# Optimization experiments

Hardware: AMD Instinct MI355X
Metric: run time of the kernel (lower is better)

The kernel has to match this reference:

```python
import jax, jax.numpy as jnp
import numpy as np

B, L, D, H = 4, 2048, 1024, 16
HD = D // H  # head_dim = 64


def setup_inputs() -> dict:
    key = jax.random.key(0)
    k1, k2, k3, k4 = jax.random.split(key, 4)
    x = jax.random.normal(k1, (B, L, D), dtype=jnp.float32)
    key_padding_mask = jax.random.randint(k2, (B, L), 0, 2) == 1
    scale = 1.0 / np.sqrt(D)
    Wqkv = jax.random.normal(k3, (3 * D, D), dtype=jnp.float32) * scale
    Wproj = jax.random.normal(k4, (D, D), dtype=jnp.float32) * scale
    return {"x": x, "key_padding_mask": key_padding_mask, "Wqkv": Wqkv, "Wproj": Wproj}


def reference(x, key_padding_mask, Wqkv, Wproj):
    b, l, d = x.shape
    qkv = jnp.einsum('bld,ed->ble', x, Wqkv)          # [B, L, 3D]
    q, k, v = jnp.split(qkv, 3, axis=-1)
    # [B, H, L, HD]
    q = q.reshape(b, l, H, HD).transpose(0, 2, 1, 3)
    k = k.reshape(b, l, H, HD).transpose(0, 2, 1, 3)
    v = v.reshape(b, l, H, HD).transpose(0, 2, 1, 3)
    scale = 1.0 / jnp.sqrt(jnp.asarray(HD, dtype=x.dtype))
    scores = jnp.einsum('bhqd,bhkd->bhqk', q, k) * scale  # [B, H, L, L]
    # key_padding_mask True = PAD -> -inf bias on key axis
    bias = jnp.where(key_padding_mask[:, None, None, :], -jnp.inf, 0.0).astype(x.dtype)
    attn = jax.nn.softmax(scores + bias, axis=-1)
    y = jnp.einsum('bhqk,bhkd->bhqd', attn, v)            # [B, H, L, HD]
    y = y.transpose(0, 2, 1, 3).reshape(b, l, d)          # [B, L, D]
    return jnp.einsum('bld,ed->ble', y, Wproj)
```

## Files before the change

### kernel.cpp

```cpp
#include <hip/hip_runtime.h>

#define L_SEQ 2048
#define DIM   1024
#define NH    16
#define HDIM  64
#define KDIM  1024

typedef short  short8 __attribute__((ext_vector_type(8)));
typedef __bf16 bf16x8 __attribute__((ext_vector_type(8)));
typedef __bf16 bf16x4 __attribute__((ext_vector_type(4)));
typedef float  f32x4  __attribute__((ext_vector_type(4)));
typedef unsigned u32x4 __attribute__((ext_vector_type(4)));

__device__ __forceinline__ unsigned short f2bf(float f) {
  unsigned u = __builtin_bit_cast(unsigned, f);
  u += 0x7fffu + ((u >> 16) & 1u);
  return (unsigned short)(u >> 16);
}

__device__ __forceinline__ void gload16(const void* g, void* l) {
  __builtin_amdgcn_global_load_lds(
      (const __attribute__((address_space(1))) void*)g,
      (__attribute__((address_space(3))) void*)l, 16, 0, 0);
}

__device__ __forceinline__ bf16x8 ldfrag(const unsigned short* p) {
  return __builtin_bit_cast(bf16x8, *(const short8*)p);
}
#define MFMA16(a, b, c) __builtin_amdgcn_mfma_f32_16x16x32_bf16(a, b, c, 0, 0, 0)

__device__ __forceinline__ unsigned cvtpk(float a, float b) {
  unsigned r;
  asm("v_cvt_pk_bf16_f32 %0, %1, %2" : "=v"(r) : "v"(a), "v"(b));
  return r;
}
__device__ __forceinline__ void xchg(unsigned &a, unsigned &b) {
  asm("v_permlane32_swap_b32 %0, %1" : "+v"(a), "+v"(b));
  asm("v_permlane16_swap_b32 %0, %1" : "+v"(a), "+v"(b));
}

__global__ __launch_bounds__(256) void cvt_bf16(const float* __restrict__ src,
                                                unsigned short* __restrict__ dst,
                                                int n) {
  int i = (blockIdx.x * 256 + threadIdx.x) * 8;
  if (i >= n) return;
  f32x4 a = *(const f32x4*)(src + i);
  f32x4 b = *(const f32x4*)(src + i + 4);
  short8 o;
  o[0] = (short)f2bf(a[0]); o[1] = (short)f2bf(a[1]);
  o[2] = (short)f2bf(a[2]); o[3] = (short)f2bf(a[3]);
  o[4] = (short)f2bf(b[0]); o[5] = (short)f2bf(b[1]);
  o[6] = (short)f2bf(b[2]); o[7] = (short)f2bf(b[3]);
  *(short8*)(dst + i) = o;
}

__global__ __launch_bounds__(256) void zero_buf(f32x4* __restrict__ dst, int n4) {
  int i = blockIdx.x * 256 + threadIdx.x;
  if (i < n4) dst[i] = f32x4{0.f, 0.f, 0.f, 0.f};
}

__global__ __launch_bounds__(256) void mask_scan(const int* __restrict__ mask,
                                                 int* __restrict__ rowl,
                                                 int* __restrict__ lc) {
  const int b = blockIdx.x, t = threadIdx.x;
  __shared__ int wsum[4];
  __shared__ int lcs;
  const int* mrow = mask + b * L_SEQ + t * 8;
  int m[8], c = 0;
#pragma unroll
  for (int i = 0; i < 8; ++i) { m[i] = mrow[i]; c += (m[i] == 0); }
  const int lane = t & 63, w = t >> 6;
  int sc = c;
#pragma unroll
  for (int d = 1; d < 64; d <<= 1) {
    int v = __shfl_up(sc, d);
    if (lane >= d) sc += v;
  }
  if (lane == 63) wsum[w] = sc;
  __syncthreads();
  int pre = sc - c;
  for (int i = 0; i < w; ++i) pre += wsum[i];
  int run = pre;
#pragma unroll
  for (int i = 0; i < 8; ++i) {
    if (m[i] == 0) { rowl[b * L_SEQ + run] = t * 8 + i; ++run; }
  }
  if (t == 255) { lc[b] = run; lcs = run; }
  __syncthreads();
  int total = lcs;
#pragma unroll
  for (int i = 0; i < 8; ++i) {
    int slot = t * 8 + i;
    if (slot >= total) rowl[b * L_SEQ + slot] = 0;
  }
}

__device__ __forceinline__ void gemm128_mainloop(
    const unsigned short* __restrict__ A, const unsigned short* __restrict__ Bt,
    const int (&asrc)[4], int n0,
    unsigned short* As0, unsigned short* As1,
    unsigned short* Bs0, unsigned short* Bs1,
    f32x4 (&acc)[4][4]) {
  const int t = threadIdx.x;
  const int lane = t & 63, wid = t >> 6;
  const int wm = wid >> 1, wn = wid & 1;
  const int lr = lane & 15, lk = (lane >> 4) * 8;
  const int swr = (lr & 7) << 3;
  constexpr int NT = KDIM / 64;

  auto stage = [&](unsigned short* Ad, unsigned short* Bd, int kt) {
#pragma unroll
    for (int i = 0; i < 4; ++i) {
      int row = i * 32 + (t >> 3);
      int cs = ((t & 7) ^ (row & 7)) * 8;
      gload16(A + (size_t)asrc[i] * KDIM + kt * 64 + cs,
              Ad + row * 64 + (t & 7) * 8);
    }
#pragma unroll
    for (int i = 0; i < 4; ++i) {
      int row = i * 32 + (t >> 3);
      int cs = ((t & 7) ^ (row & 7)) * 8;
      gload16(Bt + (size_t)(n0 + row) * KDIM + kt * 64 + cs,
              Bd + row * 64 + (t & 7) * 8);
    }
  };

  auto tile = [&](const unsigned short* Ac, const unsigned short* Bc,
                  unsigned short* An, unsigned short* Bn, int kt) {
    if (kt + 1 < NT) {
      stage(An, Bn, kt + 1);
      asm volatile("s_waitcnt vmcnt(8)" ::: "memory");
    } else {
      asm volatile("s_waitcnt vmcnt(0)" ::: "memory");
    }
    __builtin_amdgcn_sched_barrier(0);
    __builtin_amdgcn_s_barrier();
    __builtin_amdgcn_sched_barrier(0);
    bf16x8 af[4][2], bfv[4][2];
#pragma unroll
    for (int mf = 0; mf < 4; ++mf)
#pragma unroll
      for (int kh = 0; kh < 2; ++kh)
        af[mf][kh] = ldfrag(Ac + (wm * 64 + mf * 16 + lr) * 64 +
                            ((kh * 32 + lk) ^ swr));
#pragma unroll
    for (int nf = 0; nf < 4; ++nf)
#pragma unroll
      for (int kh = 0; kh < 2; ++kh)
        bfv[nf][kh] = ldfrag(Bc + (wn * 64 + nf * 16 + lr) * 64 +
                             ((kh * 32 + lk) ^ swr));
    __builtin_amdgcn_s_setprio(1);
#pragma unroll
    for (int mf = 0; mf < 4; ++mf)
#pragma unroll
      for (int nf = 0; nf < 4; ++nf) {
        acc[mf][nf] = MFMA16(af[mf][0], bfv[nf][0], acc[mf][nf]);
        acc[mf][nf] = MFMA16(af[mf][1], bfv[nf][1], acc[mf][nf]);
      }
    __builtin_amdgcn_s_setprio(0);
    __builtin_amdgcn_sched_barrier(0);
    __builtin_amdgcn_s_barrier();
  };

  stage(As0, Bs0, 0);
  for (int kt = 0; kt < NT; kt += 2) {
    tile(As0, Bs0, As1, Bs1, kt);
    tile(As1, Bs1, As0, Bs0, kt + 1);
  }
}

__global__ __launch_bounds__(256, 2) void gemm_qkv(
    const unsigned short* __restrict__ xb, const unsigned short* __restrict__ wb,
    const int* __restrict__ rowl, const int* __restrict__ lc,
    unsigned short* __restrict__ qw, unsigned short* __restrict__ kw,
    unsigned short* __restrict__ vtw) {
  __shared__ unsigned short As[2][128 * 64];
  __shared__ unsigned short Bs[2][128 * 64];
  const int nx = blockIdx.x;
  const int m0 = blockIdx.y * 128;
  const int sec = nx >> 3;
  const int n0 = nx * 128;
  const int b = m0 >> 11;
  const int lcb = lc[b];
  if (sec > 0 && (m0 & 2047) >= lcb) return;
  const int t = threadIdx.x;
  int asrc[4];
#pragma unroll
  for (int i = 0; i < 4; ++i) {
    int p = m0 + i * 32 + (t >> 3);
    asrc[i] = (sec == 0) ? p : ((p & ~2047) + rowl[p]);
  }
  f32x4 acc[4][4] = {};
  gemm128_mainloop(xb, wb, asrc, n0, As[0], As[1], Bs[0], Bs[1], acc);

  const int lane = t & 63, wid = t >> 6;
  const int wm = wid >> 1, wn = wid & 1;
  const int lr = lane & 15, g4 = (lane >> 4) * 4;
  const int nb = n0 & 1023;
  if (sec == 0) {
#pragma unroll
    for (int mf = 0; mf < 4; ++mf)
#pragma unroll
      for (int nf = 0; nf < 4; ++nf) {
        int e = nb + wn * 64 + nf * 16 + lr;
        int h = e >> 6, hd = e & 63;
#pragma unroll
        for (int r = 0; r < 4; ++r) {
          int m = m0 + wm * 64 + mf * 16 + g4 + r;
          qw[(((size_t)(b * NH + h)) * L_SEQ + (m & 2047)) * HDIM + hd] =
              f2bf(acc[mf][nf][r]);
        }
      }
  } else {
#pragma unroll
    for (int mf = 0; mf < 4; ++mf)
#pragma unroll
      for (int r = 0; r < 4; ++r) {
        int m = m0 + wm * 64 + mf * 16 + g4 + r;
        int tgt = m & 2047;
        if (tgt >= lcb) continue;
        size_t bb = (size_t)b * NH;
#pragma unroll
        for (int nf = 0; nf < 4; ++nf) {
          int e = nb + wn * 64 + nf * 16 + lr;
          int h = e >> 6, hd = e & 63;
          unsigned short val = f2bf(acc[mf][nf][r]);
          if (sec == 1) kw[((bb + h) * L_SEQ + tgt) * HDIM + hd] = val;
          else          vtw[((bb + h) * HDIM + hd) * L_SEQ + tgt] = val;
        }
      }
  }
}

__global__ __launch_bounds__(256, 2) void gemm_proj(
    const unsigned short* __restrict__ yb, const unsigned short* __restrict__ wb,
    float* __restrict__ out) {
  __shared__ unsigned short As[2][128 * 64];
  __shared__ unsigned short Bs[2][128 * 64];
  const int n0 = blockIdx.x * 128, m0 = blockIdx.y * 128;
  const int t = threadIdx.x;
  int asrc[4];
#pragma unroll
  for (int i = 0; i < 4; ++i) asrc[i] = m0 + i * 32 + (t >> 3);
  f32x4 acc[4][4] = {};
  gemm128_mainloop(yb, wb, asrc, n0, As[0], As[1], Bs[0], Bs[1], acc);
  const int lane = t & 63, wid = t >> 6;
  const int wm = wid >> 1, wn = wid & 1;
  const int lr = lane & 15, g4 = (lane >> 4) * 4;
#pragma unroll
  for (int mf = 0; mf < 4; ++mf)
#pragma unroll
    for (int nf = 0; nf < 4; ++nf) {
      int e = n0 + wn * 64 + nf * 16 + lr;
#pragma unroll
      for (int r = 0; r < 4; ++r) {
        int m = m0 + wm * 64 + mf * 16 + g4 + r;
        out[(size_t)m * DIM + e] = acc[mf][nf][r];
      }
    }
}

__global__ __launch_bounds__(256, 4) void attn_kernel(
    const unsigned short* __restrict__ qw, const unsigned short* __restrict__ kw,
    const unsigned short* __restrict__ vtw, const int* __restrict__ lc,
    unsigned short* __restrict__ yb) {
  __shared__ unsigned short Ks[2][64 * 64];
  __shared__ unsigned short Vts[2][64 * 64];
  const int bh = blockIdx.y;
  const int q0 = blockIdx.x * 128;
  const int b = bh >> 4, h = bh & 15;
  const int t = threadIdx.x, wid = t >> 6, lane = t & 63;
  const int lr = lane & 15, lk = (lane >> 4) * 8, g4 = (lane >> 4) * 4;
  const int swr = (lr & 7) << 3;
  const float KE = 0.18033688011112042f;

  const int Lcv = lc[b];
  const int nt = (Lcv + 63) >> 6;

  bf16x8 qf[2][2];
  const size_t qbase = (size_t)bh * L_SEQ + q0 + wid * 32;
#pragma unroll
  for (int qi = 0; qi < 2; ++qi)
#pragma unroll
    for (int kh = 0; kh < 2; ++kh)
      qf[qi][kh] = __builtin_bit_cast(bf16x8,
          *(const short8*)(qw + (qbase + qi * 16 + lr) * HDIM + kh * 32 + lk));

  f32x4 o[2][4] = {};
  float mrun[2] = {-3.0e38f, -3.0e38f};
  float lrun[2] = {0.f, 0.f};

  auto stage = [&](int buf, int kt) {
#pragma unroll
    for (int i = 0; i < 2; ++i) {
      int c = i * 256 + t;
      int row = c >> 3;
      int cs = ((c & 7) ^ (row & 7)) * 8;
      gload16(kw  + ((size_t)bh * L_SEQ + kt * 64 + row) * HDIM + cs, &Ks[buf][c * 8]);
      gload16(vtw + ((size_t)bh * HDIM + row) * L_SEQ + kt * 64 + cs, &Vts[buf][c * 8]);
    }
  };

  stage(0, 0);
  int cur = 0;

  for (int kt = 0; kt < nt; ++kt) {
    if (kt + 1 < nt) {
      stage(cur ^ 1, kt + 1);
      asm volatile("s_waitcnt vmcnt(4)" ::: "memory");
    } else {
      asm volatile("s_waitcnt vmcnt(0)" ::: "memory");
    }
    __builtin_amdgcn_s_barrier();
    __builtin_amdgcn_sched_barrier(0);

    const unsigned short* Kc = Ks[cur];
    f32x4 s[2][4] = {};
    __builtin_amdgcn_s_setprio(1);
#pragma unroll
    for (int nf = 0; nf < 4; ++nf) {
      bf16x8 k0 = __builtin_bit_cast(bf16x8,
          *(const short8*)(Kc + (nf * 16 + lr) * 64 + ((0 + lk) ^ swr)));
      bf16x8 k1 = __builtin_bit_cast(bf16x8,
          *(const short8*)(Kc + (nf * 16 + lr) * 64 + ((32 + lk) ^ swr)));
      s[0][nf] = MFMA16(k0, qf[0][0], s[0][nf]);
      s[0][nf] = MFMA16(k1, qf[0][1], s[0][nf]);
      s[1][nf] = MFMA16(k0, qf[1][0], s[1][nf]);
      s[1][nf] = MFMA16(k1, qf[1][1], s[1][nf]);
    }
    __builtin_amdgcn_s_setprio(0);

    if (kt == nt - 1) {
      int kbase = kt * 64 + g4;
#pragma unroll
      for (int nf = 0; nf < 4; ++nf)
#pragma unroll
        for (int r = 0; r < 4; ++r)
          if (kbase + nf * 16 + r >= Lcv) {
            s[0][nf][r] = -3.0e38f;
            s[1][nf][r] = -3.0e38f;
          }
    }

    float pmax[2];
#pragma unroll
    for (int qi = 0; qi < 2; ++qi) {
      float a0 = fmaxf(fmaxf(s[qi][0][0], s[qi][0][1]), fmaxf(s[qi][0][2], s[qi][0][3]));
      float a1 = fmaxf(fmaxf(s[qi][1][0], s[qi][1][1]), fmaxf(s[qi][1][2], s[qi][1][3]));
      float a2 = fmaxf(fmaxf(s[qi][2][0], s[qi][2][1]), fmaxf(s[qi][2][2], s[qi][2][3]));
      float a3 = fmaxf(fmaxf(s[qi][3][0], s[qi][3][1]), fmaxf(s[qi][3][2], s[qi][3][3]));
      float mm = fmaxf(fmaxf(a0, a1), fmaxf(a2, a3));
      mm = fmaxf(mm, __shfl_xor(mm, 16));
      mm = fmaxf(mm, __shfl_xor(mm, 32));
      pmax[qi] = mm;
    }

    bool need = (pmax[0] > mrun[0] + 8.0f) || (pmax[1] > mrun[1] + 8.0f);
    if (__any(need)) {
#pragma unroll
      for (int qi = 0; qi < 2; ++qi) {
        float mn = fmaxf(mrun[qi], pmax[qi]);
        float al = __builtin_amdgcn_exp2f((mrun[qi] - mn) * KE);
        mrun[qi] = mn;
        lrun[qi] *= al;
#pragma unroll
        for (int df = 0; df < 4; ++df) o[qi][df] *= al;
      }
    }

    bf16x8 pb[2][2];
#pragma unroll
    for (int qi = 0; qi < 2; ++qi) {
      float mk_ = mrun[qi] * KE;
      f32x4 rs4 = {0.f, 0.f, 0.f, 0.f};
#pragma unroll
      for (int nf = 0; nf < 4; ++nf) {
#pragma unroll
        for (int r = 0; r < 4; ++r)
          s[qi][nf][r] = __builtin_amdgcn_exp2f(s[qi][nf][r] * KE - mk_);
        rs4 += s[qi][nf];
      }
      float rsum = (rs4[0] + rs4[1]) + (rs4[2] + rs4[3]);
      rsum += __shfl_xor(rsum, 16);
      rsum += __shfl_xor(rsum, 32);
      lrun[qi] += rsum;
      unsigned w00 = cvtpk(s[qi][0][0], s[qi][0][1]);
      unsigned w01 = cvtpk(s[qi][0][2], s[qi][0][3]);
      unsigned w10 = cvtpk(s[qi][1][0], s[qi][1][1]);
      unsigned w11 = cvtpk(s[qi][1][2], s[qi][1][3]);
      unsigned w20 = cvtpk(s[qi][2][0], s[qi][2][1]);
      unsigned w21 = cvtpk(s[qi][2][2], s[qi][2][3]);
      unsigned w30 = cvtpk(s[qi][3][0], s[qi][3][1]);
      unsigned w31 = cvtpk(s[qi][3][2], s[qi][3][3]);
      xchg(w00, w10);
      xchg(w01, w11);
      xchg(w20, w30);
      xchg(w21, w31);
      u32x4 f0 = {w00, w01, w10, w11};
      u32x4 f1 = {w20, w21, w30, w31};
      pb[qi][0] = __builtin_bit_cast(bf16x8, f0);
      pb[qi][1] = __builtin_bit_cast(bf16x8, f1);
    }

    const unsigned short* Vc = Vts[cur];
    __builtin_amdgcn_s_setprio(1);
#pragma unroll
    for (int df = 0; df < 4; ++df) {
      bf16x8 v0 = __builtin_bit_cast(bf16x8,
          *(const short8*)(Vc + (df * 16 + lr) * 64 + ((0 + lk) ^ swr)));
      bf16x8 v1 = __builtin_bit_cast(bf16x8,
          *(const short8*)(Vc + (df * 16 + lr) * 64 + ((32 + lk) ^ swr)));
      o[0][df] = MFMA16(v0, pb[0][0], o[0][df]);
      o[0][df] = MFMA16(v1, pb[0][1], o[0][df]);
      o[1][df] = MFMA16(v0, pb[1][0], o[1][df]);
      o[1][df] = MFMA16(v1, pb[1][1], o[1][df]);
    }
    __builtin_amdgcn_s_setprio(0);

    __builtin_amdgcn_sched_barrier(0);
    __builtin_amdgcn_s_barrier();
    cur ^= 1;
  }

#pragma unroll
  for (int qi = 0; qi < 2; ++qi) {
    float inv = 1.0f / lrun[qi];
    int q = q0 + wid * 32 + qi * 16 + lr;
#pragma unroll
    for (int df = 0; df < 4; ++df) {
      bf16x4 pk = {(__bf16)(o[qi][df][0] * inv), (__bf16)(o[qi][df][1] * inv),
                   (__bf16)(o[qi][df][2] * inv), (__bf16)(o[qi][df][3] * inv)};
      *(bf16x4*)(yb + ((size_t)b * L_SEQ + q) * DIM + h * 64 + df * 16 + g4) = pk;
    }
  }
}

extern "C" void kernel_launch(void* const* d_in, const int* in_sizes, int n_in,
                              void* d_out, int out_size, void* d_ws, size_t ws_size,
                              hipStream_t stream) {
  const float* x     = (const float*)d_in[0];
  const int*   mask  = (const int*)d_in[1];
  const float* wqkv  = (const float*)d_in[2];
  const float* wproj = (const float*)d_in[3];
  char* ws = (char*)d_ws;
  unsigned short* xb     = (unsigned short*)(ws + 0);
  unsigned short* wqkvb  = (unsigned short*)(ws + 16777216);
  unsigned short* wprojb = (unsigned short*)(ws + 23068672);
  unsigned short* qw     = (unsigned short*)(ws + 25165824);
  unsigned short* kw     = (unsigned short*)(ws + 41943040);
  unsigned short* vtw    = (unsigned short*)(ws + 58720256);
  unsigned short* yb     = (unsigned short*)(ws + 75497472);
  int*            rowl   = (int*)(ws + 92274688);
  int*            lcArr  = (int*)(ws + 92307456);

  cvt_bf16<<<dim3(8388608 / 2048), 256, 0, stream>>>(x, xb, 8388608);
  cvt_bf16<<<dim3(3145728 / 2048), 256, 0, stream>>>(wqkv, wqkvb, 3145728);
  cvt_bf16<<<dim3(1048576 / 2048), 256, 0, stream>>>(wproj, wprojb, 1048576);
  mask_scan<<<dim3(4), 256, 0, stream>>>(mask, rowl, lcArr);
  zero_buf<<<dim3(4096), 256, 0, stream>>>((f32x4*)vtw, 1048576);
  gemm_qkv<<<dim3(24, 64), 256, 0, stream>>>(xb, wqkvb, rowl, lcArr, qw, kw, vtw);
  attn_kernel<<<dim3(16, 64), 256, 0, stream>>>(qw, kw, vtw, lcArr, yb);
  gemm_proj<<<dim3(8, 64), 256, 0, stream>>>(yb, wprojb, (float*)d_out);
}
```

Before: 166.4 us.

## Load GEMM B fragments directly from global, remap blocks across XCDs

The GEMM mainloop no longer stages the weight tile in LDS. Each wave reads its B fragments straight from global memory into registers, which halves LDS use and lets occupancy rise to 3 blocks per CU. The vmcnt waits are adjusted to count the extra in-flight loads. All three kernels also get a block-index swizzle that groups neighbouring tiles on the same XCD for L2 locality. The risk is less-coalesced global reads for B, since each lane fetches 16-byte chunks from rows spaced KDIM apart, and possible register pressure.

Result: slower. 230.9 us (+38.8%).

```diff
diff --git a/kernel.cpp b/kernel.cpp
--- a/kernel.cpp
+++ b/kernel.cpp
@@ -99,7 +99,6 @@
     const unsigned short* __restrict__ A, const unsigned short* __restrict__ Bt,
     const int (&asrc)[4], int n0,
     unsigned short* As0, unsigned short* As1,
-    unsigned short* Bs0, unsigned short* Bs1,
     f32x4 (&acc)[4][4]) {
   const int t = threadIdx.x;
   const int lane = t & 63, wid = t >> 6;
@@ -108,7 +107,9 @@
   const int swr = (lr & 7) << 3;
   constexpr int NT = KDIM / 64;
 
-  auto stage = [&](unsigned short* Ad, unsigned short* Bd, int kt) {
+  const unsigned short* bbase = Bt + (size_t)(n0 + wn * 64 + lr) * KDIM + lk;
+
+  auto stageA = [&](unsigned short* Ad, int kt) {
 #pragma unroll
     for (int i = 0; i < 4; ++i) {
       int row = i * 32 + (t >> 3);
@@ -116,39 +117,32 @@
       gload16(A + (size_t)asrc[i] * KDIM + kt * 64 + cs,
               Ad + row * 64 + (t & 7) * 8);
     }
-#pragma unroll
-    for (int i = 0; i < 4; ++i) {
-      int row = i * 32 + (t >> 3);
-      int cs = ((t & 7) ^ (row & 7)) * 8;
-      gload16(Bt + (size_t)(n0 + row) * KDIM + kt * 64 + cs,
-              Bd + row * 64 + (t & 7) * 8);
-    }
   };
 
-  auto tile = [&](const unsigned short* Ac, const unsigned short* Bc,
-                  unsigned short* An, unsigned short* Bn, int kt) {
+  auto tile = [&](const unsigned short* Ac, unsigned short* An, int kt) {
+    bf16x8 bfv[4][2];
+#pragma unroll
+    for (int nf = 0; nf < 4; ++nf)
+#pragma unroll
+      for (int kh = 0; kh < 2; ++kh)
+        bfv[nf][kh] = __builtin_bit_cast(bf16x8,
+            *(const short8*)(bbase + nf * 16 * KDIM + kt * 64 + kh * 32));
     if (kt + 1 < NT) {
-      stage(An, Bn, kt + 1);
+      stageA(An, kt + 1);
+      asm volatile("s_waitcnt vmcnt(12)" ::: "memory");
+    } else {
       asm volatile("s_waitcnt vmcnt(8)" ::: "memory");
-    } else {
-      asm volatile("s_waitcnt vmcnt(0)" ::: "memory");
     }
     __builtin_amdgcn_sched_barrier(0);
     __builtin_amdgcn_s_barrier();
     __builtin_amdgcn_sched_barrier(0);
-    bf16x8 af[4][2], bfv[4][2];
+    bf16x8 af[4][2];
 #pragma unroll
     for (int mf = 0; mf < 4; ++mf)
 #pragma unroll
       for (int kh = 0; kh < 2; ++kh)
         af[mf][kh] = ldfrag(Ac + (wm * 64 + mf * 16 + lr) * 64 +
                             ((kh * 32 + lk) ^ swr));
-#pragma unroll
-    for (int nf = 0; nf < 4; ++nf)
-#pragma unroll
-      for (int kh = 0; kh < 2; ++kh)
-        bfv[nf][kh] = ldfrag(Bc + (wn * 64 + nf * 16 + lr) * 64 +
-                             ((kh * 32 + lk) ^ swr));
     __builtin_amdgcn_s_setprio(1);
 #pragma unroll
     for (int mf = 0; mf < 4; ++mf)
@@ -162,22 +156,23 @@
     __builtin_amdgcn_s_barrier();
   };
 
-  stage(As0, Bs0, 0);
+  stageA(As0, 0);
   for (int kt = 0; kt < NT; kt += 2) {
-    tile(As0, Bs0, As1, Bs1, kt);
-    tile(As1, Bs1, As0, Bs0, kt + 1);
-  }
-}
-
-__global__ __launch_bounds__(256, 2) void gemm_qkv(
+    tile(As0, As1, kt);
+    tile(As1, As0, kt + 1);
+  }
+}
+
+__global__ __launch_bounds__(256, 3) void gemm_qkv(
     const unsigned short* __restrict__ xb, const unsigned short* __restrict__ wb,
     const int* __restrict__ rowl, const int* __restrict__ lc,
     unsigned short* __restrict__ qw, unsigned short* __restrict__ kw,
     unsigned short* __restrict__ vtw) {
   __shared__ unsigned short As[2][128 * 64];
-  __shared__ unsigned short Bs[2][128 * 64];
-  const int nx = blockIdx.x;
-  const int m0 = blockIdx.y * 128;
+  const int flat = blockIdx.x + 24 * blockIdx.y;
+  const int e = (flat & 7) * 192 + (flat >> 3);
+  const int nx = e >> 6;
+  const int m0 = (e & 63) * 128;
   const int sec = nx >> 3;
   const int n0 = nx * 128;
   const int b = m0 >> 11;
@@ -191,7 +186,7 @@
     asrc[i] = (sec == 0) ? p : ((p & ~2047) + rowl[p]);
   }
   f32x4 acc[4][4] = {};
-  gemm128_mainloop(xb, wb, asrc, n0, As[0], As[1], Bs[0], Bs[1], acc);
+  gemm128_mainloop(xb, wb, asrc, n0, As[0], As[1], acc);
 
   const int lane = t & 63, wid = t >> 6;
   const int wm = wid >> 1, wn = wid & 1;
@@ -202,8 +197,8 @@
     for (int mf = 0; mf < 4; ++mf)
 #pragma unroll
       for (int nf = 0; nf < 4; ++nf) {
-        int e = nb + wn * 64 + nf * 16 + lr;
-        int h = e >> 6, hd = e & 63;
+        int e2 = nb + wn * 64 + nf * 16 + lr;
+        int h = e2 >> 6, hd = e2 & 63;
 #pragma unroll
         for (int r = 0; r < 4; ++r) {
           int m = m0 + wm * 64 + mf * 16 + g4 + r;
@@ -222,8 +217,8 @@
         size_t bb = (size_t)b * NH;
 #pragma unroll
         for (int nf = 0; nf < 4; ++nf) {
-          int e = nb + wn * 64 + nf * 16 + lr;
-          int h = e >> 6, hd = e & 63;
+          int e2 = nb + wn * 64 + nf * 16 + lr;
+          int h = e2 >> 6, hd = e2 & 63;
           unsigned short val = f2bf(acc[mf][nf][r]);
           if (sec == 1) kw[((bb + h) * L_SEQ + tgt) * HDIM + hd] = val;
           else          vtw[((bb + h) * HDIM + hd) * L_SEQ + tgt] = val;
@@ -232,18 +227,20 @@
   }
 }
 
-__global__ __launch_bounds__(256, 2) void gemm_proj(
+__global__ __launch_bounds__(256, 3) void gemm_proj(
     const unsigned short* __restrict__ yb, const unsigned short* __restrict__ wb,
     float* __restrict__ out) {
   __shared__ unsigned short As[2][128 * 64];
-  __shared__ unsigned short Bs[2][128 * 64];
-  const int n0 = blockIdx.x * 128, m0 = blockIdx.y * 128;
+  const int flat = blockIdx.x + 8 * blockIdx.y;
+  const int e = (flat & 7) * 64 + (flat >> 3);
+  const int n0 = (e >> 6) * 128;
+  const int m0 = (e & 63) * 128;
   const int t = threadIdx.x;
   int asrc[4];
 #pragma unroll
   for (int i = 0; i < 4; ++i) asrc[i] = m0 + i * 32 + (t >> 3);
   f32x4 acc[4][4] = {};
-  gemm128_mainloop(yb, wb, asrc, n0, As[0], As[1], Bs[0], Bs[1], acc);
+  gemm128_mainloop(yb, wb, asrc, n0, As[0], As[1], acc);
   const int lane = t & 63, wid = t >> 6;
   const int wm = wid >> 1, wn = wid & 1;
   const int lr = lane & 15, g4 = (lane >> 4) * 4;
@@ -251,11 +248,11 @@
   for (int mf = 0; mf < 4; ++mf)
 #pragma unroll
     for (int nf = 0; nf < 4; ++nf) {
-      int e = n0 + wn * 64 + nf * 16 + lr;
+      int e2 = n0 + wn * 64 + nf * 16 + lr;
 #pragma unroll
       for (int r = 0; r < 4; ++r) {
         int m = m0 + wm * 64 + mf * 16 + g4 + r;
-        out[(size_t)m * DIM + e] = acc[mf][nf][r];
+        out[(size_t)m * DIM + e2] = acc[mf][nf][r];
       }
     }
 }
@@ -266,8 +263,10 @@
     unsigned short* __restrict__ yb) {
   __shared__ unsigned short Ks[2][64 * 64];
   __shared__ unsigned short Vts[2][64 * 64];
-  const int bh = blockIdx.y;
-  const int q0 = blockIdx.x * 128;
+  const int flat = blockIdx.x + 16 * blockIdx.y;
+  const int e = (flat & 7) * 128 + (flat >> 3);
+  const int bh = e >> 4;
+  const int q0 = (e & 15) * 128;
   const int b = bh >> 4, h = bh & 15;
   const int t = threadIdx.x, wid = t >> 6, lane = t & 63;
   const int lr = lane & 15, lk = (lane >> 4) * 8, g4 = (lane >> 4) * 4;
```
